# Kernel tuning notes

Measured on AMD Instinct MI355X. Metric: run time of the kernel, lower is better.

The kernel has to match this reference:

```python
import jax, jax.numpy as jnp
import numpy as np

N_TOKENS = 65536
D_MODEL = 256
D_HID = 256
N_EXPERTS = 8


def setup_inputs() -> dict:
    key = jax.random.key(0)
    ks = jax.random.split(key, 6)
    x = jax.random.normal(ks[0], (N_TOKENS, D_MODEL), dtype=jnp.float32)
    # gate Linear weight [E, d] (torch Linear stores [out, in]); small init like nn.Linear default scale
    wg = jax.random.normal(ks[1], (N_EXPERTS, D_MODEL), dtype=jnp.float32) * 0.06
    W1 = jax.random.normal(ks[2], (N_EXPERTS, D_MODEL, D_HID), dtype=jnp.float32) * 0.06
    b1 = jnp.zeros((N_EXPERTS, D_HID), dtype=jnp.float32)
    W2 = jax.random.normal(ks[3], (N_EXPERTS, D_HID, D_MODEL), dtype=jnp.float32) * 0.06
    b2 = jnp.zeros((N_EXPERTS, D_MODEL), dtype=jnp.float32)
    return {"x": x, "wg": wg, "W1": W1, "b1": b1, "W2": W2, "b2": b2}


def reference(x, wg, W1, b1, W2, b2):
    # Gate: logits = x @ wg.T ; softmax over experts ; top-1 gate value + assignment
    gates = jax.nn.softmax(x @ wg.T, axis=1)                  # [N, E]
    gate_val = jnp.max(gates, axis=1)                          # [N] == topk(k=1) values
    assign = jnp.argmax(gates, axis=1)                         # [N] expert id per token

    out = jnp.zeros_like(x)
    # Fixed small loop over experts (structural, not data-dim); each iter is one dense GEMM pair.
    for e in range(N_EXPERTS):
        h = jax.nn.relu(x @ W1[e] + b1[e])                     # [N, D_HID]
        y_e = h @ W2[e] + b2[e]                                # [N, D_MODEL]
        sel = (assign == e)[:, None]
        out = jnp.where(sel, y_e * gate_val[:, None], out)
    return out
```

## Files before the change

### kernel.cpp

```cpp
#include <hip/hip_runtime.h>
#include <hip/hip_bf16.h>
#include <math.h>

#define NTOK 65536
#define DMODEL 256
#define NEXP 8
#define CAP 65536
#define MAXTILES 1040
#define CSTRIDE 64

typedef __bf16 bf16_t;
typedef __bf16 bf16x8 __attribute__((ext_vector_type(8)));
typedef float f32x4 __attribute__((ext_vector_type(4)));

__device__ inline void async16(const void* g, void* l) {
  __builtin_amdgcn_global_load_lds(
      (const __attribute__((address_space(1))) unsigned int*)g,
      (__attribute__((address_space(3))) unsigned int*)l, 16, 0, 0);
}

__global__ __launch_bounds__(256) void gate_pack_kernel(
    const float* __restrict__ x, const float* __restrict__ wg,
    const float* __restrict__ W1, const float* __restrict__ W2,
    bf16_t* __restrict__ xb, float* __restrict__ gateval,
    int* __restrict__ counts, int* __restrict__ idxbuf,
    bf16_t* __restrict__ w1p, bf16_t* __restrict__ w2p) {
  __shared__ __align__(16) float xs[64 * 128];
  __shared__ double part[3][64][9];
  const int th = threadIdx.x;
  const int lane = th & 63;
  const int wv = th >> 6;
  const int tokbase = blockIdx.x * 64;
  const int xm = lane & 31;
  double acc[8] = {0, 0, 0, 0, 0, 0, 0, 0};

#pragma unroll
  for (int i = 0; i < 8; ++i) {
    int p = i * 256 + th;
    int r = p >> 5, c = (p & 31) ^ (r & 31);
    async16(x + (size_t)(tokbase + r) * 256 + c * 4, &xs[(i * 256 + wv * 64) * 4]);
  }
#pragma unroll
  for (int jj = 0; jj < 2; ++jj) {
    int f = blockIdx.x * 2 + jj;
    int mat = f >> 10, e = (f >> 7) & 7, kf = (f >> 4) & 7, nt = f & 15;
    const float* src = (mat == 0 ? W1 : W2) + (size_t)e * 65536;
    bf16_t* dst = (mat == 0 ? w1p : w2p) + (((size_t)e * 8 + kf) * 16 + nt) * 512;
#pragma unroll
    for (int rep = 0; rep < 2; ++rep) {
      int kl = rep * 16 + (th >> 4), nl = th & 15;
      float v = src[(size_t)(kf * 32 + kl) * 256 + nt * 16 + nl];
      int lanep = nl + 16 * (kl >> 3), j = kl & 7;
      dst[lanep * 8 + j] = (bf16_t)v;
    }
  }
  __syncthreads();

#pragma unroll
  for (int h = 0; h < 2; ++h) {
#pragma unroll
    for (int i = 0; i < 4; ++i) {
      int p = i * 256 + th;
      int r = p >> 4, cb = p & 15, mk = r & 31;
      f32x4 a = *(const f32x4*)&xs[r * 128 + (((2 * cb) ^ mk) * 4)];
      f32x4 b = *(const f32x4*)&xs[r * 128 + (((2 * cb + 1) ^ mk) * 4)];
      bf16x8 bv;
      bv[0] = (bf16_t)a[0]; bv[1] = (bf16_t)a[1];
      bv[2] = (bf16_t)a[2]; bv[3] = (bf16_t)a[3];
      bv[4] = (bf16_t)b[0]; bv[5] = (bf16_t)b[1];
      bv[6] = (bf16_t)b[2]; bv[7] = (bf16_t)b[3];
      *(bf16x8*)(xb + (size_t)(tokbase + r) * 256 + h * 128 + cb * 8) = bv;
    }
#pragma unroll
    for (int g = 0; g < 4; ++g) {
      int c0 = wv * 8 + 2 * g;
      f32x4 a = *(const f32x4*)&xs[lane * 128 + ((c0 ^ xm) * 4)];
      f32x4 b = *(const f32x4*)&xs[lane * 128 + (((c0 + 1) ^ xm) * 4)];
      float xv[8] = {a[0], a[1], a[2], a[3], b[0], b[1], b[2], b[3]};
#pragma unroll
      for (int e = 0; e < 8; ++e) {
        const float* wge = wg + e * 256 + h * 128 + wv * 32 + g * 8;
        float s = 0.f;
#pragma unroll
        for (int j2 = 0; j2 < 8; ++j2) s = fmaf(xv[j2], wge[j2], s);
        acc[e] += (double)s;
      }
    }
    if (h == 0) {
      __syncthreads();
#pragma unroll
      for (int i = 0; i < 8; ++i) {
        int p = i * 256 + th;
        int r = p >> 5, c = (p & 31) ^ (r & 31);
        async16(x + (size_t)(tokbase + r) * 256 + 128 + c * 4, &xs[(i * 256 + wv * 64) * 4]);
      }
      __syncthreads();
    }
  }

  if (wv > 0) {
#pragma unroll
    for (int e = 0; e < 8; ++e) part[wv - 1][lane][e] = acc[e];
  }
  __syncthreads();
  if (wv == 0) {
#pragma unroll
    for (int s2 = 0; s2 < 3; ++s2)
#pragma unroll
      for (int e = 0; e < 8; ++e) acc[e] += part[s2][lane][e];
    double m = acc[0]; int bi = 0;
#pragma unroll
    for (int e = 1; e < 8; ++e) if (acc[e] > m) { m = acc[e]; bi = e; }
    float denom = 0.f;
#pragma unroll
    for (int e = 0; e < 8; ++e) denom += __expf((float)(acc[e] - m));
    const int tok = tokbase + lane;
    gateval[tok] = 1.0f / denom;
    unsigned long long mymask = 0;
#pragma unroll
    for (int e = 0; e < NEXP; ++e) {
      unsigned long long mk = __ballot(bi == e);
      if (lane == e) mymask = mk;
    }
    int mybase = 0;
    if (lane < NEXP) mybase = atomicAdd(&counts[lane * CSTRIDE], (int)__popcll(mymask));
#pragma unroll
    for (int e = 0; e < NEXP; ++e) {
      unsigned long long mk = __ballot(bi == e);
      int b = __shfl(mybase, e, 64);
      if (bi == e) {
        int pos = b + (int)__popcll(mk & ((1ull << lane) - 1ull));
        idxbuf[e * CAP + pos] = tok;
      }
    }
  }
}

__global__ __launch_bounds__(512, 4) void moe_gemm_kernel(
    const bf16_t* __restrict__ xb, const bf16_t* __restrict__ w1p,
    const bf16_t* __restrict__ w2p, const float* __restrict__ b1,
    const float* __restrict__ b2, const float* __restrict__ gateval,
    const int* __restrict__ counts, const int* __restrict__ idxbuf,
    float* __restrict__ out) {
  int ex = -1, tm = 0, a2 = 0, cnte = 0;
#pragma unroll
  for (int e2 = 0; e2 < 8; ++e2) {
    int c = counts[e2 * CSTRIDE];
    int n = (c + 63) >> 6;
    if ((int)blockIdx.x >= a2 && (int)blockIdx.x < a2 + n) {
      ex = e2; tm = (int)blockIdx.x - a2; cnte = c;
    }
    a2 += n;
  }
  if (ex < 0) return;
  const int ccnt = cnte;
  __shared__ __align__(16) bf16_t ts[64 * 256];
  __shared__ int sidx[64];
  __shared__ float sgv[64];
  const int th = threadIdx.x;
  const int lane = th & 63, wv = th >> 6;
  const int lr = lane & 15, lq = lane >> 4;
  if (th < 64) {
    int r = tm * 64 + th;
    int t = idxbuf[ex * CAP + (r < ccnt ? r : ccnt - 1)];
    sidx[th] = t;
    sgv[th] = gateval[t];
  }
  __syncthreads();
#pragma unroll
  for (int i = 0; i < 4; ++i) {
    int p = i * 512 + th;
    int r = p >> 5, s = (p & 31) ^ (r & 31);
    async16(xb + (size_t)sidx[r] * 256 + s * 8, &ts[(i * 512 + wv * 64) * 8]);
  }
  __syncthreads();

  const bf16_t* w1e = w1p + (size_t)ex * 65536;
  {
    f32x4 acc[4][2] = {};
#pragma unroll
    for (int kk = 0; kk < 256; kk += 64) {
#pragma unroll
      for (int kb = 0; kb < 2; ++kb) {
        const int ks = (kk >> 3) + kb * 4 + lq;
        const int kf = (kk >> 5) + kb;
        bf16x8 af[4], bfr[2];
#pragma unroll
        for (int mi = 0; mi < 4; ++mi) {
          int r = mi * 16 + lr;
          af[mi] = *(const bf16x8*)&ts[(r * 32 + (ks ^ (r & 31))) * 8];
        }
#pragma unroll
        for (int ni = 0; ni < 2; ++ni)
          bfr[ni] = *(const bf16x8*)&w1e[((size_t)kf * 16 + wv * 2 + ni) * 512 + lane * 8];
#pragma unroll
        for (int mi = 0; mi < 4; ++mi)
#pragma unroll
          for (int ni = 0; ni < 2; ++ni)
            acc[mi][ni] = __builtin_amdgcn_mfma_f32_16x16x32_bf16(af[mi], bfr[ni], acc[mi][ni], 0, 0, 0);
      }
    }
    float b1v[2];
#pragma unroll
    for (int ni = 0; ni < 2; ++ni) b1v[ni] = b1[ex * 256 + wv * 32 + ni * 16 + lr];
    __syncthreads();
#pragma unroll
    for (int mi = 0; mi < 4; ++mi)
#pragma unroll
      for (int ni = 0; ni < 2; ++ni)
#pragma unroll
        for (int rr = 0; rr < 4; ++rr) {
          int m = mi * 16 + lq * 4 + rr;
          int n = wv * 32 + ni * 16 + lr;
          float v = acc[mi][ni][rr] + b1v[ni];
          v = v > 0.f ? v : 0.f;
          ts[(m * 32 + ((n >> 3) ^ (m & 31))) * 8 + (n & 7)] = (bf16_t)v;
        }
  }
  __syncthreads();

  const bf16_t* w2e = w2p + (size_t)ex * 65536;
  {
    f32x4 acc[4][2] = {};
#pragma unroll
    for (int kk = 0; kk < 256; kk += 64) {
#pragma unroll
      for (int kb = 0; kb < 2; ++kb) {
        const int ks = (kk >> 3) + kb * 4 + lq;
        const int kf = (kk >> 5) + kb;
        bf16x8 af[4], bfr[2];
#pragma unroll
        for (int mi = 0; mi < 4; ++mi) {
          int r = mi * 16 + lr;
          af[mi] = *(const bf16x8*)&ts[(r * 32 + (ks ^ (r & 31))) * 8];
        }
#pragma unroll
        for (int ni = 0; ni < 2; ++ni)
          bfr[ni] = *(const bf16x8*)&w2e[((size_t)kf * 16 + wv * 2 + ni) * 512 + lane * 8];
#pragma unroll
        for (int mi = 0; mi < 4; ++mi)
#pragma unroll
          for (int ni = 0; ni < 2; ++ni)
            acc[mi][ni] = __builtin_amdgcn_mfma_f32_16x16x32_bf16(af[mi], bfr[ni], acc[mi][ni], 0, 0, 0);
      }
    }
    float b2v[2];
#pragma unroll
    for (int ni = 0; ni < 2; ++ni) b2v[ni] = b2[ex * 256 + wv * 32 + ni * 16 + lr];
#pragma unroll
    for (int mi = 0; mi < 4; ++mi)
#pragma unroll
      for (int rr = 0; rr < 4; ++rr) {
        int m = mi * 16 + lq * 4 + rr;
        int row = tm * 64 + m;
        if (row < ccnt) {
          int tk = sidx[m];
          float g = sgv[m];
#pragma unroll
          for (int ni = 0; ni < 2; ++ni) {
            int n = wv * 32 + ni * 16 + lr;
            out[(size_t)tk * 256 + n] = (acc[mi][ni][rr] + b2v[ni]) * g;
          }
        }
      }
  }
}

extern "C" void kernel_launch(void* const* d_in, const int* in_sizes, int n_in,
                              void* d_out, int out_size, void* d_ws, size_t ws_size,
                              hipStream_t stream) {
  (void)in_sizes; (void)n_in; (void)out_size; (void)ws_size;
  const float* x  = (const float*)d_in[0];
  const float* wg = (const float*)d_in[1];
  const float* W1 = (const float*)d_in[2];
  const float* b1 = (const float*)d_in[3];
  const float* W2 = (const float*)d_in[4];
  const float* b2 = (const float*)d_in[5];
  float* out = (float*)d_out;

  char* ws = (char*)d_ws;
  size_t off = 0;
  auto alloc = [&](size_t bytes) {
    void* p = ws + off;
    off += (bytes + 255) & ~(size_t)255;
    return p;
  };
  bf16_t* xb     = (bf16_t*)alloc((size_t)NTOK * DMODEL * 2);
  bf16_t* w1p    = (bf16_t*)alloc((size_t)NEXP * 256 * 256 * 2);
  bf16_t* w2p    = (bf16_t*)alloc((size_t)NEXP * 256 * 256 * 2);
  int*    idxbuf = (int*)alloc((size_t)NEXP * CAP * 4);
  float*  gv     = (float*)alloc((size_t)NTOK * 4);
  int*    counts = (int*)alloc((size_t)NEXP * CSTRIDE * 4);

  hipMemsetAsync(counts, 0, (size_t)NEXP * CSTRIDE * 4, stream);
  hipLaunchKernelGGL(gate_pack_kernel, dim3(NTOK / 64), dim3(256), 0, stream,
                     x, wg, W1, W2, xb, gv, counts, idxbuf, w1p, w2p);
  hipLaunchKernelGGL(moe_gemm_kernel, dim3(MAXTILES), dim3(512), 0, stream,
                     xb, w1p, w2p, b1, b2, gv, counts, idxbuf, out);
}
```

Baseline: 173.3 us.

## Double-buffer gate x staging over 128 tokens and vectorize MoE output stores via LDS

The gate kernel now handles 128 tokens per block and double-buffers the x half-tiles in LDS, so the next async load is issued while the current one is converted and dotted. It also halves the number of counter atomics per token. The GEMM epilogue writes results into LDS and then stores contiguous 16-byte vectors to the scattered output rows instead of scalar strided stores. This adds extra barriers and reuses the tile LDS, and the gate grid is halved, which lowers parallelism.

```diff
diff --git a/kernel.cpp b/kernel.cpp
--- a/kernel.cpp
+++ b/kernel.cpp
@@ -25,24 +25,28 @@
     bf16_t* __restrict__ xb, float* __restrict__ gateval,
     int* __restrict__ counts, int* __restrict__ idxbuf,
     bf16_t* __restrict__ w1p, bf16_t* __restrict__ w2p) {
-  __shared__ __align__(16) float xs[64 * 128];
+  __shared__ __align__(16) float xs[2][64 * 128];
   __shared__ double part[3][64][9];
   const int th = threadIdx.x;
   const int lane = th & 63;
   const int wv = th >> 6;
-  const int tokbase = blockIdx.x * 64;
+  const int tokbase = blockIdx.x * 128;
   const int xm = lane & 31;
-  double acc[8] = {0, 0, 0, 0, 0, 0, 0, 0};
-
-#pragma unroll
-  for (int i = 0; i < 8; ++i) {
-    int p = i * 256 + th;
-    int r = p >> 5, c = (p & 31) ^ (r & 31);
-    async16(x + (size_t)(tokbase + r) * 256 + c * 4, &xs[(i * 256 + wv * 64) * 4]);
-  }
-#pragma unroll
-  for (int jj = 0; jj < 2; ++jj) {
-    int f = blockIdx.x * 2 + jj;
+
+  auto stage = [&](int u) {
+#pragma unroll
+    for (int i = 0; i < 8; ++i) {
+      int p = i * 256 + th;
+      int r = p >> 5, c = (p & 31) ^ (r & 31);
+      async16(x + (size_t)(tokbase + (u >> 1) * 64 + r) * 256 + (u & 1) * 128 + c * 4,
+              &xs[u & 1][(i * 256 + wv * 64) * 4]);
+    }
+  };
+
+  stage(0);
+#pragma unroll
+  for (int jj = 0; jj < 4; ++jj) {
+    int f = blockIdx.x * 4 + jj;
     int mat = f >> 10, e = (f >> 7) & 7, kf = (f >> 4) & 7, nt = f & 15;
     const float* src = (mat == 0 ? W1 : W2) + (size_t)e * 65536;
     bf16_t* dst = (mat == 0 ? w1p : w2p) + (((size_t)e * 8 + kf) * 16 + nt) * 512;
@@ -56,26 +60,31 @@
   }
   __syncthreads();
 
-#pragma unroll
-  for (int h = 0; h < 2; ++h) {
+  int bi0 = 0, bi1 = 0;
+  double acc[8] = {0, 0, 0, 0, 0, 0, 0, 0};
+#pragma unroll
+  for (int u = 0; u < 4; ++u) {
+    if (u < 3) stage(u + 1);
+    const float* xh = xs[u & 1];
+    const int h = u & 1, ps = u >> 1;
 #pragma unroll
     for (int i = 0; i < 4; ++i) {
       int p = i * 256 + th;
       int r = p >> 4, cb = p & 15, mk = r & 31;
-      f32x4 a = *(const f32x4*)&xs[r * 128 + (((2 * cb) ^ mk) * 4)];
-      f32x4 b = *(const f32x4*)&xs[r * 128 + (((2 * cb + 1) ^ mk) * 4)];
+      f32x4 a = *(const f32x4*)&xh[r * 128 + (((2 * cb) ^ mk) * 4)];
+      f32x4 b = *(const f32x4*)&xh[r * 128 + (((2 * cb + 1) ^ mk) * 4)];
       bf16x8 bv;
       bv[0] = (bf16_t)a[0]; bv[1] = (bf16_t)a[1];
       bv[2] = (bf16_t)a[2]; bv[3] = (bf16_t)a[3];
       bv[4] = (bf16_t)b[0]; bv[5] = (bf16_t)b[1];
       bv[6] = (bf16_t)b[2]; bv[7] = (bf16_t)b[3];
-      *(bf16x8*)(xb + (size_t)(tokbase + r) * 256 + h * 128 + cb * 8) = bv;
+      *(bf16x8*)(xb + (size_t)(tokbase + ps * 64 + r) * 256 + h * 128 + cb * 8) = bv;
     }
 #pragma unroll
     for (int g = 0; g < 4; ++g) {
       int c0 = wv * 8 + 2 * g;
-      f32x4 a = *(const f32x4*)&xs[lane * 128 + ((c0 ^ xm) * 4)];
-      f32x4 b = *(const f32x4*)&xs[lane * 128 + (((c0 + 1) ^ xm) * 4)];
+      f32x4 a = *(const f32x4*)&xh[lane * 128 + ((c0 ^ xm) * 4)];
+      f32x4 b = *(const f32x4*)&xh[lane * 128 + (((c0 + 1) ^ xm) * 4)];
       float xv[8] = {a[0], a[1], a[2], a[3], b[0], b[1], b[2], b[3]};
 #pragma unroll
       for (int e = 0; e < 8; ++e) {
@@ -86,52 +95,58 @@
         acc[e] += (double)s;
       }
     }
-    if (h == 0) {
+    if (u & 1) {
+      if (wv > 0) {
+#pragma unroll
+        for (int e = 0; e < 8; ++e) part[wv - 1][lane][e] = acc[e];
+      }
       __syncthreads();
-#pragma unroll
-      for (int i = 0; i < 8; ++i) {
-        int p = i * 256 + th;
-        int r = p >> 5, c = (p & 31) ^ (r & 31);
-        async16(x + (size_t)(tokbase + r) * 256 + 128 + c * 4, &xs[(i * 256 + wv * 64) * 4]);
-      }
+      if (wv == 0) {
+        double a2[8];
+#pragma unroll
+        for (int e = 0; e < 8; ++e) a2[e] = acc[e];
+#pragma unroll
+        for (int s2 = 0; s2 < 3; ++s2)
+#pragma unroll
+          for (int e = 0; e < 8; ++e) a2[e] += part[s2][lane][e];
+        double m = a2[0]; int bi = 0;
+#pragma unroll
+        for (int e = 1; e < 8; ++e) if (a2[e] > m) { m = a2[e]; bi = e; }
+        float denom = 0.f;
+#pragma unroll
+        for (int e = 0; e < 8; ++e) denom += __expf((float)(a2[e] - m));
+        gateval[tokbase + ps * 64 + lane] = 1.0f / denom;
+        if (ps == 0) bi0 = bi; else bi1 = bi;
+      }
+#pragma unroll
+      for (int e = 0; e < 8; ++e) acc[e] = 0.0;
       __syncthreads();
-    }
-  }
-
-  if (wv > 0) {
-#pragma unroll
-    for (int e = 0; e < 8; ++e) part[wv - 1][lane][e] = acc[e];
-  }
-  __syncthreads();
+    } else {
+      __syncthreads();
+    }
+  }
+
   if (wv == 0) {
-#pragma unroll
-    for (int s2 = 0; s2 < 3; ++s2)
-#pragma unroll
-      for (int e = 0; e < 8; ++e) acc[e] += part[s2][lane][e];
-    double m = acc[0]; int bi = 0;
-#pragma unroll
-    for (int e = 1; e < 8; ++e) if (acc[e] > m) { m = acc[e]; bi = e; }
-    float denom = 0.f;
-#pragma unroll
-    for (int e = 0; e < 8; ++e) denom += __expf((float)(acc[e] - m));
-    const int tok = tokbase + lane;
-    gateval[tok] = 1.0f / denom;
-    unsigned long long mymask = 0;
+    const unsigned long long below = (1ull << lane) - 1ull;
+    int myc = 0;
 #pragma unroll
     for (int e = 0; e < NEXP; ++e) {
-      unsigned long long mk = __ballot(bi == e);
-      if (lane == e) mymask = mk;
+      unsigned long long mk0 = __ballot(bi0 == e);
+      unsigned long long mk1 = __ballot(bi1 == e);
+      if (lane == e) myc = (int)__popcll(mk0) + (int)__popcll(mk1);
     }
     int mybase = 0;
-    if (lane < NEXP) mybase = atomicAdd(&counts[lane * CSTRIDE], (int)__popcll(mymask));
+    if (lane < NEXP) mybase = atomicAdd(&counts[lane * CSTRIDE], myc);
 #pragma unroll
     for (int e = 0; e < NEXP; ++e) {
-      unsigned long long mk = __ballot(bi == e);
-      int b = __shfl(mybase, e, 64);
-      if (bi == e) {
-        int pos = b + (int)__popcll(mk & ((1ull << lane) - 1ull));
-        idxbuf[e * CAP + pos] = tok;
-      }
+      unsigned long long mk0 = __ballot(bi0 == e);
+      unsigned long long mk1 = __ballot(bi1 == e);
+      int b0 = __shfl(mybase, e, 64);
+      if (bi0 == e)
+        idxbuf[e * CAP + b0 + (int)__popcll(mk0 & below)] = tokbase + lane;
+      if (bi1 == e)
+        idxbuf[e * CAP + b0 + (int)__popcll(mk0) + (int)__popcll(mk1 & below)] =
+            tokbase + 64 + lane;
     }
   }
 }
@@ -247,22 +262,37 @@
     float b2v[2];
 #pragma unroll
     for (int ni = 0; ni < 2; ++ni) b2v[ni] = b2[ex * 256 + wv * 32 + ni * 16 + lr];
-#pragma unroll
-    for (int mi = 0; mi < 4; ++mi)
-#pragma unroll
-      for (int rr = 0; rr < 4; ++rr) {
-        int m = mi * 16 + lq * 4 + rr;
+    __syncthreads();
+    float* wb = (float*)&ts[0] + wv * 1024;
+#pragma unroll
+    for (int bt = 0; bt < 2; ++bt) {
+#pragma unroll
+      for (int mi2 = 0; mi2 < 2; ++mi2) {
+        const int mi = bt * 2 + mi2;
+#pragma unroll
+        for (int ni = 0; ni < 2; ++ni)
+#pragma unroll
+          for (int rr = 0; rr < 4; ++rr) {
+            int lm = mi2 * 16 + lq * 4 + rr;
+            int lc = ni * 16 + lr;
+            int m = mi * 16 + lq * 4 + rr;
+            float v = (acc[mi][ni][rr] + b2v[ni]) * sgv[m];
+            int slot = ((lc >> 2) + (lm & 7)) & 7;
+            wb[lm * 32 + slot * 4 + (lc & 3)] = v;
+          }
+      }
+#pragma unroll
+      for (int rd = 0; rd < 4; ++rd) {
+        int lm = rd * 8 + (lane >> 3);
+        int kk2 = lane & 7;
+        int slot = (kk2 + (lm & 7)) & 7;
+        f32x4 v = *(const f32x4*)&wb[lm * 32 + slot * 4];
+        int m = bt * 32 + lm;
         int row = tm * 64 + m;
-        if (row < ccnt) {
-          int tk = sidx[m];
-          float g = sgv[m];
-#pragma unroll
-          for (int ni = 0; ni < 2; ++ni) {
-            int n = wv * 32 + ni * 16 + lr;
-            out[(size_t)tk * 256 + n] = (acc[mi][ni][rr] + b2v[ni]) * g;
-          }
-        }
-      }
+        if (row < ccnt)
+          *(f32x4*)&out[(size_t)sidx[m] * 256 + wv * 32 + kk2 * 4] = v;
+      }
+    }
   }
 }
 
@@ -293,7 +323,7 @@
   int*    counts = (int*)alloc((size_t)NEXP * CSTRIDE * 4);
 
   hipMemsetAsync(counts, 0, (size_t)NEXP * CSTRIDE * 4, stream);
-  hipLaunchKernelGGL(gate_pack_kernel, dim3(NTOK / 64), dim3(256), 0, stream,
+  hipLaunchKernelGGL(gate_pack_kernel, dim3(NTOK / 128), dim3(256), 0, stream,
                      x, wg, W1, W2, xb, gv, counts, idxbuf, w1p, w2p);
   hipLaunchKernelGGL(moe_gemm_kernel, dim3(MAXTILES), dim3(512), 0, stream,
                      xb, w1p, w2p, b1, b2, gv, counts, idxbuf, out);
```

New measurement: 173.5 us. About the same (+0.1%).
